# Optimization experiments

Measured on AMD Instinct MI355X. Metric: run time of the kernel, lower is better.

## Reference

```python
import jax, jax.numpy as jnp
import numpy as np

BATCH, IN, HID, NCLS = 4096, 2048, 8192, 1000

def setup_inputs() -> dict:
    key = jax.random.key(0)
    kx, kk, kg = jax.random.split(key, 3)
    x = jax.random.normal(kx, (BATCH, IN), dtype=jnp.float32)
    # torch nn.Linear weights: kohonen [HID, IN], grossberg [NCLS, HID], init U(-1, 1)
    Wk = jax.random.uniform(kk, (HID, IN), dtype=jnp.float32, minval=-1.0, maxval=1.0)
    Wg = jax.random.uniform(kg, (NCLS, HID), dtype=jnp.float32, minval=-1.0, maxval=1.0)
    return {"x": x, "Wk": Wk, "Wg": Wg}

def reference(x, Wk, Wg):
    # L2-normalize each row
    xn = x / jnp.linalg.norm(x, axis=1, keepdims=True)  # [B, IN]
    kohonen_out = jnp.einsum('bi,hi->bh', xn, Wk)        # [B, HID]
    idx = jnp.argmax(kohonen_out, axis=1)                # [B] winner units
    # one-hot @ Wg.T == gather columns of Wg for winning units
    out = jnp.take(Wg, idx, axis=1).T                    # [B, NCLS]
    return out
```

## Files before the change

### kernel.cpp

```cpp
#include <hip/hip_runtime.h>
#include <stdint.h>

typedef unsigned int u32;
typedef unsigned long long u64;
typedef unsigned short u16;
typedef unsigned char u8;
typedef int intx8 __attribute__((ext_vector_type(8)));
typedef float floatx4 __attribute__((ext_vector_type(4)));

#define BATCH 4096
#define IN    2048
#define HID   8192
#define NCLS  1000

#define OFF_ROWKEY 0u
#define OFF_TOPK   32768u
#define OFF_X8     16809984u
#define OFF_WK8    25198592u
#define OFF_WGT    41975808u
#define TOTAL_FULL 74743808ull

__device__ __forceinline__ u32 fkey(float f) {
    u32 u = __float_as_uint(f);
    return (u & 0x80000000u) ? ~u : (u | 0x80000000u);
}
__device__ __forceinline__ float unfkey(u32 k) {
    return __uint_as_float((k & 0x80000000u) ? (k ^ 0x80000000u) : ~k);
}
__device__ __forceinline__ void ce(u64& a, u64& b) {
    u64 mx = a > b ? a : b;
    u64 mn = a > b ? b : a;
    a = mx; b = mn;
}

__global__ __launch_bounds__(256) void prep_kernel(
    const float* __restrict__ x, const float* __restrict__ Wk,
    const float* __restrict__ Wg,
    u8* __restrict__ x8, u8* __restrict__ wk8, float* __restrict__ WgT)
{
    __shared__ float t[32][33];
    const int bid = blockIdx.x;
    if (bid < 1024) {
        const int gid = bid * 256 + threadIdx.x;
        const int NSX = BATCH * IN / 16;
        const int NS  = NSX + HID * IN / 16;
        for (int s = gid; s < NS; s += 1024 * 256) {
            const float4* src; u8* dst;
            if (s < NSX) { src = (const float4*)x + (size_t)s * 4;  dst = x8  + (size_t)s * 16; }
            else { int u = s - NSX; src = (const float4*)Wk + (size_t)u * 4; dst = wk8 + (size_t)u * 16; }
            uint4 o;
            float4 f;
            int p;
            f = src[0];
            p = __builtin_amdgcn_cvt_pk_fp8_f32(f.x, f.y, 0, false);
            p = __builtin_amdgcn_cvt_pk_fp8_f32(f.z, f.w, p, true);  o.x = (u32)p;
            f = src[1];
            p = __builtin_amdgcn_cvt_pk_fp8_f32(f.x, f.y, 0, false);
            p = __builtin_amdgcn_cvt_pk_fp8_f32(f.z, f.w, p, true);  o.y = (u32)p;
            f = src[2];
            p = __builtin_amdgcn_cvt_pk_fp8_f32(f.x, f.y, 0, false);
            p = __builtin_amdgcn_cvt_pk_fp8_f32(f.z, f.w, p, true);  o.z = (u32)p;
            f = src[3];
            p = __builtin_amdgcn_cvt_pk_fp8_f32(f.x, f.y, 0, false);
            p = __builtin_amdgcn_cvt_pk_fp8_f32(f.z, f.w, p, true);  o.w = (u32)p;
            *(uint4*)dst = o;
        }
    } else {
        const int tb = bid - 1024;
        const int bx = (tb & 255) * 32;
        const int by = (tb >> 8) * 32;
        const int tx = threadIdx.x & 31, ty = threadIdx.x >> 5;
        #pragma unroll
        for (int i = 0; i < 32; i += 8) {
            int c = by + ty + i;
            t[ty + i][tx] = (c < NCLS) ? Wg[(size_t)c * HID + bx + tx] : 0.f;
        }
        __syncthreads();
        #pragma unroll
        for (int i = 0; i < 32; i += 8) {
            int c = by + tx;
            if (c < NCLS) WgT[(size_t)(bx + ty + i) * NCLS + by + tx] = t[tx][ty + i];
        }
    }
}

__global__ __launch_bounds__(256) void mfma_fp8_gemm_kernel(
    const u8* __restrict__ x8, const u8* __restrict__ wk8,
    u64* __restrict__ topk)
{
    __shared__ __align__(16) u8 At[128 * 128];
    __shared__ __align__(16) u8 Bt[128 * 128];

    const int tid  = threadIdx.x;
    const int lane = tid & 63;
    const int w    = tid >> 6;
    const int bm   = blockIdx.y * 128;
    const int bn   = blockIdx.x * 128;
    const int wrow = (w >> 1) * 64, wcol = (w & 1) * 64;
    const int m = lane & 15, q = lane >> 4;

    floatx4 acc[4][4];
    #pragma unroll
    for (int i = 0; i < 4; i++)
        #pragma unroll
        for (int j = 0; j < 4; j++)
            acc[i][j] = (floatx4){0.f, 0.f, 0.f, 0.f};

    const int srow = tid >> 3;
    const int soff = (((((tid >> 1) & 3) ^ (srow & 3)) * 2) + (tid & 1)) * 16;
    const u8* gxa = x8  + (size_t)(bm + srow) * IN + soff;
    const u8* gwb = wk8 + (size_t)(bn + srow) * IN + soff;

    const int foq = (q ^ (m & 3)) * 32;

    #pragma unroll 1
    for (int k0 = 0; k0 < IN; k0 += 128) {
        #pragma unroll
        for (int s = 0; s < 4; s++) {
            __builtin_amdgcn_global_load_lds(
                (const __attribute__((address_space(1))) u32*)(gxa + k0 + (size_t)s * 32 * IN),
                (__attribute__((address_space(3))) u32*)&At[s * 4096 + tid * 16], 16, 0, 0);
            __builtin_amdgcn_global_load_lds(
                (const __attribute__((address_space(1))) u32*)(gwb + k0 + (size_t)s * 32 * IN),
                (__attribute__((address_space(3))) u32*)&Bt[s * 4096 + tid * 16], 16, 0, 0);
        }
        __syncthreads();

        intx8 af[4];
        #pragma unroll
        for (int i = 0; i < 4; i++)
            af[i] = *(const intx8*)&At[(wrow + i * 16 + m) * 128 + foq];
        #pragma unroll
        for (int j = 0; j < 4; j++) {
            intx8 bf = *(const intx8*)&Bt[(wcol + j * 16 + m) * 128 + foq];
            #pragma unroll
            for (int i = 0; i < 4; i++)
                acc[i][j] = __builtin_amdgcn_mfma_scale_f32_16x16x128_f8f6f4(
                    af[i], bf, acc[i][j],
                    0, 0,
                    0, 0x7F,
                    0, 0x7F);
        }

        __syncthreads();
    }

    const int g4 = (blockIdx.x * 2 + (wcol >> 6)) * 4;
    #pragma unroll
    for (int i = 0; i < 4; i++) {
        #pragma unroll
        for (int r = 0; r < 4; r++) {
            u64 k0, k1, k2, k3;
            {
                const int c0 = bn + wcol + 0 * 16 + m;
                const int c1 = bn + wcol + 1 * 16 + m;
                const int c2 = bn + wcol + 2 * 16 + m;
                const int c3 = bn + wcol + 3 * 16 + m;
                k0 = ((u64)fkey(acc[i][0][r]) << 32) | (u64)(0x1FFFu - (u32)c0);
                k1 = ((u64)fkey(acc[i][1][r]) << 32) | (u64)(0x1FFFu - (u32)c1);
                k2 = ((u64)fkey(acc[i][2][r]) << 32) | (u64)(0x1FFFu - (u32)c2);
                k3 = ((u64)fkey(acc[i][3][r]) << 32) | (u64)(0x1FFFu - (u32)c3);
            }
            ce(k0, k1); ce(k2, k3); ce(k0, k2); ce(k1, k3); ce(k1, k2);
            #pragma unroll
            for (int off = 1; off < 16; off <<= 1) {
                u64 b0 = __shfl_xor(k0, off, 64);
                u64 b1 = __shfl_xor(k1, off, 64);
                u64 b2 = __shfl_xor(k2, off, 64);
                u64 b3 = __shfl_xor(k3, off, 64);
                k0 = k0 > b3 ? k0 : b3;
                k1 = k1 > b2 ? k1 : b2;
                k2 = k2 > b1 ? k2 : b1;
                k3 = k3 > b0 ? k3 : b0;
                ce(k0, k2); ce(k1, k3); ce(k0, k1); ce(k2, k3);
            }
            if (m == 0) {
                const int grow = bm + wrow + i * 16 + q * 4 + r;
                ulonglong2 v01; v01.x = k0; v01.y = k1;
                ulonglong2 v23; v23.x = k2; v23.y = k3;
                *(ulonglong2*)&topk[(size_t)grow * 512 + g4]     = v01;
                *(ulonglong2*)&topk[(size_t)grow * 512 + g4 + 2] = v23;
            }
        }
    }
}

__global__ __launch_bounds__(256) void scan_kernel(
    const u64* __restrict__ topk,
    const float* __restrict__ x, const float* __restrict__ Wk,
    const float* __restrict__ WgT, float* __restrict__ out)
{
    __shared__ u64 wmax[4];
    __shared__ int cnt;
    __shared__ u64 candk[128];
    __shared__ u64 bestk;
    const int row  = blockIdx.x;
    const int tid  = threadIdx.x;
    const int lane = tid & 63;
    const int w    = tid >> 6;
    if (tid == 0) { cnt = 0; bestk = 0ull; }

    ulonglong2 kk = *(const ulonglong2*)&topk[(size_t)row * 512 + tid * 2];
    u64 mx = kk.x > kk.y ? kk.x : kk.y;
    #pragma unroll
    for (int off = 1; off < 64; off <<= 1) {
        u64 o = __shfl_xor(mx, off, 64);
        if (o > mx) mx = o;
    }
    if (lane == 0) wmax[w] = mx;
    __syncthreads();
    u64 gmax = wmax[0];
    #pragma unroll
    for (int i = 1; i < 4; i++) if (wmax[i] > gmax) gmax = wmax[i];

    const float thr = unfkey((u32)(gmax >> 32)) - 12.0f;
    if (unfkey((u32)(kk.x >> 32)) >= thr) { int c = atomicAdd(&cnt, 1); if (c < 128) candk[c] = kk.x; }
    if (unfkey((u32)(kk.y >> 32)) >= thr) { int c = atomicAdd(&cnt, 1); if (c < 128) candk[c] = kk.y; }
    __syncthreads();
    const int n = min(cnt, 128);

    int col;
    if (n <= 1) {
        col = 0x1FFF - (int)(gmax & 0xFFFFu);
    } else {
        const float4* xr = (const float4*)(x + (size_t)row * IN);
        for (int c = w; c < n; c += 4) {
            const int h = 0x1FFF - (int)(candk[c] & 0xFFFFu);
            const float4* wr = (const float4*)(Wk + (size_t)h * IN);
            float p = 0.f;
            #pragma unroll
            for (int pass = 0; pass < 8; pass++) {
                float4 a = xr[pass * 64 + lane];
                float4 b = wr[pass * 64 + lane];
                p += a.x * b.x + a.y * b.y + a.z * b.z + a.w * b.w;
            }
            #pragma unroll
            for (int off = 1; off < 64; off <<= 1) p += __shfl_xor(p, off, 64);
            if (lane == 0) {
                u64 key = ((u64)fkey(p) << 32) | (u64)(0x1FFFu - (u32)h);
                atomicMax(&bestk, key);
            }
        }
        __syncthreads();
        col = 0x1FFF - (int)(bestk & 0xFFFFu);
    }

    const float* src = WgT + (size_t)col * NCLS;
    for (int c = tid; c < NCLS; c += 256)
        out[(size_t)row * NCLS + c] = src[c];
}

__global__ void init_ws_kernel(u64* rowkey) {
    int i = blockIdx.x * blockDim.x + threadIdx.x;
    if (i < BATCH) rowkey[i] = 0ULL;
}

__global__ __launch_bounds__(256) void gemm_argmax_kernel(
    const float* __restrict__ x, const float* __restrict__ Wk,
    u64* __restrict__ rowkey)
{
    __shared__ __align__(16) float As[32 * 64];
    __shared__ __align__(16) float Bs[32 * 64];
    const int tid = threadIdx.x;
    const int bm = blockIdx.y * 64, bn = blockIdx.x * 64;
    const int tx = tid & 15, ty = tid >> 4;
    float acc[4][4];
    #pragma unroll
    for (int i = 0; i < 4; i++)
        #pragma unroll
        for (int j = 0; j < 4; j++) acc[i][j] = 0.f;
    const int r0 = tid >> 3, q0 = tid & 7;
    const int r1 = (tid + 256) >> 3, q1 = (tid + 256) & 7;
    const float* xA0 = &x[(size_t)(bm + r0) * IN + q0 * 4];
    const float* xA1 = &x[(size_t)(bm + r1) * IN + q1 * 4];
    const float* wB0 = &Wk[(size_t)(bn + r0) * IN + q0 * 4];
    const float* wB1 = &Wk[(size_t)(bn + r1) * IN + q1 * 4];
    for (int k0 = 0; k0 < IN; k0 += 32) {
        float4 a0 = *(const float4*)(xA0 + k0);
        float4 a1 = *(const float4*)(xA1 + k0);
        float4 b0 = *(const float4*)(wB0 + k0);
        float4 b1 = *(const float4*)(wB1 + k0);
        __syncthreads();
        As[(q0 * 4 + 0) * 64 + r0] = a0.x; As[(q0 * 4 + 1) * 64 + r0] = a0.y;
        As[(q0 * 4 + 2) * 64 + r0] = a0.z; As[(q0 * 4 + 3) * 64 + r0] = a0.w;
        As[(q1 * 4 + 0) * 64 + r1] = a1.x; As[(q1 * 4 + 1) * 64 + r1] = a1.y;
        As[(q1 * 4 + 2) * 64 + r1] = a1.z; As[(q1 * 4 + 3) * 64 + r1] = a1.w;
        Bs[(q0 * 4 + 0) * 64 + r0] = b0.x; Bs[(q0 * 4 + 1) * 64 + r0] = b0.y;
        Bs[(q0 * 4 + 2) * 64 + r0] = b0.z; Bs[(q0 * 4 + 3) * 64 + r0] = b0.w;
        Bs[(q1 * 4 + 0) * 64 + r1] = b1.x; Bs[(q1 * 4 + 1) * 64 + r1] = b1.y;
        Bs[(q1 * 4 + 2) * 64 + r1] = b1.z; Bs[(q1 * 4 + 3) * 64 + r1] = b1.w;
        __syncthreads();
        #pragma unroll
        for (int k = 0; k < 32; k++) {
            float4 av = *(const float4*)&As[k * 64 + ty * 4];
            float4 bv = *(const float4*)&Bs[k * 64 + tx * 4];
            acc[0][0] += av.x * bv.x; acc[0][1] += av.x * bv.y;
            acc[0][2] += av.x * bv.z; acc[0][3] += av.x * bv.w;
            acc[1][0] += av.y * bv.x; acc[1][1] += av.y * bv.y;
            acc[1][2] += av.y * bv.z; acc[1][3] += av.y * bv.w;
            acc[2][0] += av.z * bv.x; acc[2][1] += av.z * bv.y;
            acc[2][2] += av.z * bv.z; acc[2][3] += av.z * bv.w;
            acc[3][0] += av.w * bv.x; acc[3][1] += av.w * bv.y;
            acc[3][2] += av.w * bv.z; acc[3][3] += av.w * bv.w;
        }
    }
    #pragma unroll
    for (int i = 0; i < 4; i++) {
        const int row = bm + ty * 4 + i;
        u64 best = 0ULL;
        #pragma unroll
        for (int j = 0; j < 4; j++) {
            const int col = bn + tx * 4 + j;
            u64 p = ((u64)fkey(acc[i][j]) << 32) | (u64)(0x1FFFu - (unsigned)col);
            if (p > best) best = p;
        }
        #pragma unroll
        for (int off = 1; off < 16; off <<= 1) {
            u64 other = __shfl_xor(best, off, 64);
            if (other > best) best = other;
        }
        if (tx == 0) atomicMax(&rowkey[row], best);
    }
}

__global__ __launch_bounds__(256) void gather_kernel(
    const u64* __restrict__ rowkey, const float* __restrict__ Wg,
    float* __restrict__ out)
{
    const int b = blockIdx.y;
    const int c = blockIdx.x * 256 + threadIdx.x;
    if (c >= NCLS) return;
    const int col = 0x1FFF - (int)(rowkey[b] & 0xFFFFFFFFu);
    out[(size_t)b * NCLS + c] = Wg[(size_t)c * HID + col];
}

extern "C" void kernel_launch(void* const* d_in, const int* in_sizes, int n_in,
                              void* d_out, int out_size, void* d_ws, size_t ws_size,
                              hipStream_t stream) {
    const float* x  = (const float*)d_in[0];
    const float* Wk = (const float*)d_in[1];
    const float* Wg = (const float*)d_in[2];
    float* out = (float*)d_out;
    char* ws = (char*)d_ws;

    if (ws_size >= TOTAL_FULL) {
        u64* topk  = (u64*)(ws + OFF_TOPK);
        u8*  x8    = (u8*)(ws + OFF_X8);
        u8*  wk8   = (u8*)(ws + OFF_WK8);
        float* WgT = (float*)(ws + OFF_WGT);

        hipLaunchKernelGGL(prep_kernel, dim3(1024 + 8192), dim3(256), 0, stream,
                           x, Wk, Wg, x8, wk8, WgT);
        hipLaunchKernelGGL(mfma_fp8_gemm_kernel, dim3(HID / 128, BATCH / 128), dim3(256), 0, stream,
                           x8, wk8, topk);
        hipLaunchKernelGGL(scan_kernel, dim3(BATCH), dim3(256), 0, stream,
                           topk, x, Wk, WgT, out);
    } else {
        u64* rowkey = (u64*)(ws + OFF_ROWKEY);
        hipLaunchKernelGGL(init_ws_kernel, dim3(16), dim3(256), 0, stream, rowkey);
        hipLaunchKernelGGL(gemm_argmax_kernel, dim3(HID / 64, BATCH / 64), dim3(256), 0, stream,
                           x, Wk, rowkey);
        hipLaunchKernelGGL(gather_kernel, dim3(4, BATCH), dim3(256), 0, stream,
                           rowkey, Wg, out);
    }
}
```

Measured before the change: 317.6 us.

## Pack top-k candidate keys into 32-bit words and rescore one row per wave

```diff
diff --git a/kernel.cpp b/kernel.cpp
--- a/kernel.cpp
+++ b/kernel.cpp
@@ -15,10 +15,10 @@
 
 #define OFF_ROWKEY 0u
 #define OFF_TOPK   32768u
-#define OFF_X8     16809984u
-#define OFF_WK8    25198592u
-#define OFF_WGT    41975808u
-#define TOTAL_FULL 74743808ull
+#define OFF_X8     8421376u
+#define OFF_WK8    16809984u
+#define OFF_WGT    33587200u
+#define TOTAL_FULL 66355200ull
 
 __device__ __forceinline__ u32 fkey(float f) {
     u32 u = __float_as_uint(f);
@@ -26,6 +26,11 @@
 }
 __device__ __forceinline__ float unfkey(u32 k) {
     return __uint_as_float((k & 0x80000000u) ? (k ^ 0x80000000u) : ~k);
+}
+__device__ __forceinline__ void ce32(u32& a, u32& b) {
+    u32 mx = a > b ? a : b;
+    u32 mn = a > b ? b : a;
+    a = mx; b = mn;
 }
 __device__ __forceinline__ void ce(u64& a, u64& b) {
     u64 mx = a > b ? a : b;
@@ -86,7 +91,7 @@
 
 __global__ __launch_bounds__(256) void mfma_fp8_gemm_kernel(
     const u8* __restrict__ x8, const u8* __restrict__ wk8,
-    u64* __restrict__ topk)
+    u32* __restrict__ topk)
 {
     __shared__ __align__(16) u8 At[128 * 128];
     __shared__ __align__(16) u8 Bt[128 * 128];
@@ -145,109 +150,107 @@
         __syncthreads();
     }
 
-    const int g4 = (blockIdx.x * 2 + (wcol >> 6)) * 4;
+    const int group = blockIdx.x * 2 + (wcol >> 6);
     #pragma unroll
     for (int i = 0; i < 4; i++) {
         #pragma unroll
         for (int r = 0; r < 4; r++) {
-            u64 k0, k1, k2, k3;
-            {
-                const int c0 = bn + wcol + 0 * 16 + m;
-                const int c1 = bn + wcol + 1 * 16 + m;
-                const int c2 = bn + wcol + 2 * 16 + m;
-                const int c3 = bn + wcol + 3 * 16 + m;
-                k0 = ((u64)fkey(acc[i][0][r]) << 32) | (u64)(0x1FFFu - (u32)c0);
-                k1 = ((u64)fkey(acc[i][1][r]) << 32) | (u64)(0x1FFFu - (u32)c1);
-                k2 = ((u64)fkey(acc[i][2][r]) << 32) | (u64)(0x1FFFu - (u32)c2);
-                k3 = ((u64)fkey(acc[i][3][r]) << 32) | (u64)(0x1FFFu - (u32)c3);
-            }
-            ce(k0, k1); ce(k2, k3); ce(k0, k2); ce(k1, k3); ce(k1, k2);
+            u32 k0 = (fkey(acc[i][0][r]) & 0xFFFFFFC0u) | (0u << 4) | (u32)m;
+            u32 k1 = (fkey(acc[i][1][r]) & 0xFFFFFFC0u) | (1u << 4) | (u32)m;
+            u32 k2 = (fkey(acc[i][2][r]) & 0xFFFFFFC0u) | (2u << 4) | (u32)m;
+            u32 k3 = (fkey(acc[i][3][r]) & 0xFFFFFFC0u) | (3u << 4) | (u32)m;
+            ce32(k0, k1); ce32(k2, k3); ce32(k0, k2); ce32(k1, k3); ce32(k1, k2);
             #pragma unroll
             for (int off = 1; off < 16; off <<= 1) {
-                u64 b0 = __shfl_xor(k0, off, 64);
-                u64 b1 = __shfl_xor(k1, off, 64);
-                u64 b2 = __shfl_xor(k2, off, 64);
-                u64 b3 = __shfl_xor(k3, off, 64);
-                k0 = k0 > b3 ? k0 : b3;
-                k1 = k1 > b2 ? k1 : b2;
-                k2 = k2 > b1 ? k2 : b1;
-                k3 = k3 > b0 ? k3 : b0;
-                ce(k0, k2); ce(k1, k3); ce(k0, k1); ce(k2, k3);
+                u32 b0 = __shfl_xor(k0, off, 64);
+                u32 b1 = __shfl_xor(k1, off, 64);
+                u32 b2 = __shfl_xor(k2, off, 64);
+                u32 b3 = __shfl_xor(k3, off, 64);
+                u32 t0 = k0 > b3 ? k0 : b3;
+                u32 t1 = k1 > b2 ? k1 : b2;
+                u32 t2 = k2 > b1 ? k2 : b1;
+                u32 t3 = k3 > b0 ? k3 : b0;
+                ce32(t0, t2); ce32(t1, t3); ce32(t0, t1); ce32(t2, t3);
+                k0 = t0; k1 = t1; k2 = t2; k3 = t3;
             }
             if (m == 0) {
                 const int grow = bm + wrow + i * 16 + q * 4 + r;
-                ulonglong2 v01; v01.x = k0; v01.y = k1;
-                ulonglong2 v23; v23.x = k2; v23.y = k3;
-                *(ulonglong2*)&topk[(size_t)grow * 512 + g4]     = v01;
-                *(ulonglong2*)&topk[(size_t)grow * 512 + g4 + 2] = v23;
+                uint4 v; v.x = k0; v.y = k1; v.z = k2; v.w = k3;
+                *(uint4*)&topk[(size_t)grow * 512 + group * 4] = v;
             }
         }
     }
 }
 
 __global__ __launch_bounds__(256) void scan_kernel(
-    const u64* __restrict__ topk,
+    const u32* __restrict__ topk,
     const float* __restrict__ x, const float* __restrict__ Wk,
     const float* __restrict__ WgT, float* __restrict__ out)
 {
-    __shared__ u64 wmax[4];
-    __shared__ int cnt;
-    __shared__ u64 candk[128];
-    __shared__ u64 bestk;
-    const int row  = blockIdx.x;
-    const int tid  = threadIdx.x;
-    const int lane = tid & 63;
-    const int w    = tid >> 6;
-    if (tid == 0) { cnt = 0; bestk = 0ull; }
-
-    ulonglong2 kk = *(const ulonglong2*)&topk[(size_t)row * 512 + tid * 2];
-    u64 mx = kk.x > kk.y ? kk.x : kk.y;
+    __shared__ u16 cand[4][48];
+    const int wv   = threadIdx.x >> 6;
+    const int lane = threadIdx.x & 63;
+    const int row  = blockIdx.x * 4 + wv;
+
+    const uint4* tp = (const uint4*)(topk + (size_t)row * 512);
+    uint4 v0 = tp[lane];
+    uint4 v1 = tp[lane + 64];
+
+    u32 mx = v0.x > v1.x ? v0.x : v1.x;
     #pragma unroll
     for (int off = 1; off < 64; off <<= 1) {
-        u64 o = __shfl_xor(mx, off, 64);
+        u32 o = __shfl_xor(mx, off, 64);
         if (o > mx) mx = o;
     }
-    if (lane == 0) wmax[w] = mx;
-    __syncthreads();
-    u64 gmax = wmax[0];
-    #pragma unroll
-    for (int i = 1; i < 4; i++) if (wmax[i] > gmax) gmax = wmax[i];
-
-    const float thr = unfkey((u32)(gmax >> 32)) - 12.0f;
-    if (unfkey((u32)(kk.x >> 32)) >= thr) { int c = atomicAdd(&cnt, 1); if (c < 128) candk[c] = kk.x; }
-    if (unfkey((u32)(kk.y >> 32)) >= thr) { int c = atomicAdd(&cnt, 1); if (c < 128) candk[c] = kk.y; }
-    __syncthreads();
-    const int n = min(cnt, 128);
+    const float thr = unfkey(mx & 0xFFFFFFC0u) - 12.0f;
+
+    int base = 0;
+    const u32 ks[8] = {v0.x, v0.y, v0.z, v0.w, v1.x, v1.y, v1.z, v1.w};
+    #pragma unroll
+    for (int s = 0; s < 8; s++) {
+        const int group = (s < 4) ? lane : (lane + 64);
+        const u32 key = ks[s];
+        const bool in = unfkey(key & 0xFFFFFFC0u) >= thr;
+        const u64 msk = __ballot(in);
+        if (in) {
+            int rnk = base + __popcll(msk & ((1ull << lane) - 1ull));
+            if (rnk < 48)
+                cand[wv][rnk] = (u16)(group * 64 + (int)((key >> 4) & 3u) * 16 + (int)(key & 15u));
+        }
+        base += __popcll(msk);
+    }
+    const int n = min(base, 48);
+    __builtin_amdgcn_wave_barrier();
 
     int col;
     if (n <= 1) {
-        col = 0x1FFF - (int)(gmax & 0xFFFFu);
+        col = cand[wv][0];
     } else {
         const float4* xr = (const float4*)(x + (size_t)row * IN);
-        for (int c = w; c < n; c += 4) {
-            const int h = 0x1FFF - (int)(candk[c] & 0xFFFFu);
+        float4 a[8];
+        #pragma unroll
+        for (int p = 0; p < 8; p++) a[p] = xr[p * 64 + lane];
+        u64 best = 0ull;
+        for (int c = 0; c < n; c++) {
+            const int h = cand[wv][c];
             const float4* wr = (const float4*)(Wk + (size_t)h * IN);
-            float p = 0.f;
+            float s = 0.f;
             #pragma unroll
-            for (int pass = 0; pass < 8; pass++) {
-                float4 a = xr[pass * 64 + lane];
-                float4 b = wr[pass * 64 + lane];
-                p += a.x * b.x + a.y * b.y + a.z * b.z + a.w * b.w;
+            for (int p = 0; p < 8; p++) {
+                float4 b = wr[p * 64 + lane];
+                s += a[p].x * b.x + a[p].y * b.y + a[p].z * b.z + a[p].w * b.w;
             }
             #pragma unroll
-            for (int off = 1; off < 64; off <<= 1) p += __shfl_xor(p, off, 64);
-            if (lane == 0) {
-                u64 key = ((u64)fkey(p) << 32) | (u64)(0x1FFFu - (u32)h);
-                atomicMax(&bestk, key);
-            }
-        }
-        __syncthreads();
-        col = 0x1FFF - (int)(bestk & 0xFFFFu);
-    }
-
-    const float* src = WgT + (size_t)col * NCLS;
-    for (int c = tid; c < NCLS; c += 256)
-        out[(size_t)row * NCLS + c] = src[c];
+            for (int off = 1; off < 64; off <<= 1) s += __shfl_xor(s, off, 64);
+            u64 key = ((u64)fkey(s) << 32) | (u64)(0x1FFFu - (u32)h);
+            if (key > best) best = key;
+        }
+        col = 0x1FFF - (int)(best & 0xFFFFu);
+    }
+
+    const float4* src = (const float4*)(WgT + (size_t)col * NCLS);
+    float4* dst = (float4*)(out + (size_t)row * NCLS);
+    for (int t = lane; t < NCLS / 4; t += 64) dst[t] = src[t];
 }
 
 __global__ void init_ws_kernel(u64* rowkey) {
@@ -344,7 +347,7 @@
     char* ws = (char*)d_ws;
 
     if (ws_size >= TOTAL_FULL) {
-        u64* topk  = (u64*)(ws + OFF_TOPK);
+        u32* topk  = (u32*)(ws + OFF_TOPK);
         u8*  x8    = (u8*)(ws + OFF_X8);
         u8*  wk8   = (u8*)(ws + OFF_WK8);
         float* WgT = (float*)(ws + OFF_WGT);
@@ -353,7 +356,7 @@
                            x, Wk, Wg, x8, wk8, WgT);
         hipLaunchKernelGGL(mfma_fp8_gemm_kernel, dim3(HID / 128, BATCH / 128), dim3(256), 0, stream,
                            x8, wk8, topk);
-        hipLaunchKernelGGL(scan_kernel, dim3(BATCH), dim3(256), 0, stream,
+        hipLaunchKernelGGL(scan_kernel, dim3(BATCH / 4), dim3(256), 0, stream,
                            topk, x, Wk, WgT, out);
     } else {
         u64* rowkey = (u64*)(ws + OFF_ROWKEY);
```

Measured after the change: 310.3 us. 1.02x faster.
